# Kernel tuning notes

Hardware: AMD Instinct MI355X
Metric: run time of the kernel (lower is better)

Reference implementation:

```python
import jax, jax.numpy as jnp
import numpy as np

N_NODES = 50000
N_EDGES = 1600000
IN_DIM = 128
HID = 64
H1 = 2          # heads layer 0
H2 = 1          # heads layer 1
N_CLS = 16
NEG_SLOPE = 0.2


def setup_inputs() -> dict:
    key = jax.random.key(0)
    ks = jax.random.split(key, 10)
    h = jax.random.normal(ks[0], (N_NODES, IN_DIM), dtype=jnp.float32)
    src = jax.random.randint(ks[1], (N_EDGES,), 0, N_NODES, dtype=jnp.int64)
    dst = jax.random.randint(ks[2], (N_EDGES,), 0, N_NODES, dtype=jnp.int64)
    s = 0.05
    W1_src = jax.random.normal(ks[3], (IN_DIM, H1 * HID), dtype=jnp.float32) * s
    W1_dst = jax.random.normal(ks[4], (IN_DIM, H1 * HID), dtype=jnp.float32) * s
    a1 = jax.random.normal(ks[5], (H1, HID), dtype=jnp.float32) * s
    W2_src = jax.random.normal(ks[6], (H1 * HID, H2 * N_CLS), dtype=jnp.float32) * s
    W2_dst = jax.random.normal(ks[7], (H1 * HID, H2 * N_CLS), dtype=jnp.float32) * s
    a2 = jax.random.normal(ks[8], (H2, N_CLS), dtype=jnp.float32) * s
    W_res = jax.random.normal(ks[9], (H1 * HID, H2 * N_CLS), dtype=jnp.float32) * s
    return {"h": h, "src": src, "dst": dst, "W1_src": W1_src, "W1_dst": W1_dst,
            "a1": a1, "W2_src": W2_src, "W2_dst": W2_dst, "a2": a2, "W_res": W_res}


def _gatv2_conv(h, src, dst, W_src, W_dst, attn, n_nodes):
    # GATv2: e_ij = a . LeakyReLU(W_src h_j + W_dst h_i), softmax over in-edges of i
    heads, out_dim = attn.shape
    fs = (h @ W_src).reshape(-1, heads, out_dim)  # [N,H,D]
    fd = (h @ W_dst).reshape(-1, heads, out_dim)
    e = jax.nn.leaky_relu(fs[src] + fd[dst], negative_slope=NEG_SLOPE)  # [E,H,D]
    score = jnp.einsum('ehd,hd->eh', e, attn)                           # [E,H]
    m = jax.ops.segment_max(score, dst, num_segments=n_nodes)           # [N,H]
    ex = jnp.exp(score - m[dst])
    denom = jax.ops.segment_sum(ex, dst, num_segments=n_nodes)          # [N,H]
    alpha = ex / denom[dst]                                             # [E,H]
    msg = alpha[:, :, None] * fs[src]                                   # [E,H,D]
    return jax.ops.segment_sum(msg, dst, num_segments=n_nodes)          # [N,H,D]


def reference(h, src, dst, W1_src, W1_dst, a1, W2_src, W2_dst, a2, W_res):
    n = h.shape[0]
    # layer 0: GATv2Conv -> elu activation -> flatten heads
    h1 = _gatv2_conv(h, src, dst, W1_src, W1_dst, a1, n)   # [N,H1,HID]
    h1 = jax.nn.elu(h1).reshape(n, -1)                      # [N,H1*HID]
    # layer 1: GATv2Conv with residual, no activation, mean over heads
    h2 = _gatv2_conv(h1, src, dst, W2_src, W2_dst, a2, n)   # [N,H2,N_CLS]
    res = (h1 @ W_res).reshape(n, H2, N_CLS)
    logits = (h2 + res).mean(axis=1)                        # [N,N_CLS]
    return logits
```

## Files before the change

### kernel.cpp

```cpp
#include <hip/hip_runtime.h>
#include <hip/hip_bf16.h>

#define NEG 0.2f
#define FNEG_MAX -3.402823466e38f

__device__ __forceinline__ unsigned short f2bf(float f){
  unsigned u = __float_as_uint(f);
  return (unsigned short)((u + 0x7fffu + ((u >> 16) & 1u)) >> 16);
}
__device__ __forceinline__ unsigned pk2bf(float a, float b){
  return (unsigned)f2bf(a) | ((unsigned)f2bf(b) << 16);
}
__device__ __forceinline__ float bflo(unsigned u){ return __uint_as_float(u << 16); }
__device__ __forceinline__ float bfhi(unsigned u){ return __uint_as_float(u & 0xffff0000u); }

__global__ __launch_bounds__(256)
void k_count(const int* __restrict__ dst, int* __restrict__ deg, int ne){
  int e = blockIdx.x*256 + threadIdx.x;
  if (e < ne) atomicAdd(&deg[dst[e]], 1);
}

#define SCB 512
__global__ __launch_bounds__(SCB)
void k_scan1(const int* __restrict__ deg, int* __restrict__ off,
             int* __restrict__ bsum, int n){
  __shared__ int lds[SCB];
  int t = threadIdx.x, i = blockIdx.x*SCB + t;
  int x = (i < n) ? deg[i] : 0;
  lds[t] = x; __syncthreads();
  for (int s = 1; s < SCB; s <<= 1){
    int v = (t >= s) ? lds[t-s] : 0;
    __syncthreads();
    lds[t] += v;
    __syncthreads();
  }
  if (i < n) off[i] = lds[t] - x;
  if (t == SCB-1) bsum[blockIdx.x] = lds[t];
}

__global__ void k_scan2(int* __restrict__ bsum, int nblk){
  if (threadIdx.x == 0 && blockIdx.x == 0){
    int acc = 0;
    for (int b = 0; b < nblk; ++b){ int v = bsum[b]; bsum[b] = acc; acc += v; }
  }
}

__global__ __launch_bounds__(SCB)
void k_scan3(int* __restrict__ off, const int* __restrict__ bsum, int n, int ne){
  int i = blockIdx.x*SCB + threadIdx.x;
  if (i < n) off[i] += bsum[blockIdx.x];
  if (i == 0) off[n] = ne;
}

__global__ __launch_bounds__(256)
void k_scatter(const int* __restrict__ src, const int* __restrict__ dst,
               const int* __restrict__ off, int* __restrict__ cur,
               int* __restrict__ csr_src, int ne){
  int e = blockIdx.x*256 + threadIdx.x;
  if (e >= ne) return;
  int d = dst[e];
  int pos = off[d] + atomicAdd(&cur[d], 1);
  csr_src[pos] = src[e];
}

#define GM1 32
__global__ __launch_bounds__(256)
void k_gemm1(const float* __restrict__ h, const float* __restrict__ Ws,
             const float* __restrict__ Wd, unsigned* __restrict__ fs,
             float* __restrict__ fd, int n){
  __shared__ float ht[128][36];
  int tid = threadIdx.x;
  int node0 = blockIdx.x * GM1;
  for (int i = tid; i < GM1*128; i += 256){
    int r = i >> 7, c = i & 127;
    int nd = node0 + r;
    ht[c][r] = (nd < n) ? h[(size_t)nd*128 + c] : 0.f;
  }
  __syncthreads();
  int cg  = tid & 31;
  int mat = (tid >> 5) & 1;
  int q   = tid >> 6;
  const float4* W4 = (const float4*)(mat ? Wd : Ws);
  float acc[8][4];
  #pragma unroll
  for (int j = 0; j < 8; ++j){ acc[j][0]=0.f; acc[j][1]=0.f; acc[j][2]=0.f; acc[j][3]=0.f; }
  for (int k = 0; k < 128; ++k){
    float4 w = W4[k*32 + cg];
    const float4* hp4 = (const float4*)&ht[k][q*8];
    float4 ha = hp4[0], hb = hp4[1];
    float hv[8] = {ha.x, ha.y, ha.z, ha.w, hb.x, hb.y, hb.z, hb.w};
    #pragma unroll
    for (int j = 0; j < 8; ++j){
      acc[j][0] = fmaf(hv[j], w.x, acc[j][0]);
      acc[j][1] = fmaf(hv[j], w.y, acc[j][1]);
      acc[j][2] = fmaf(hv[j], w.z, acc[j][2]);
      acc[j][3] = fmaf(hv[j], w.w, acc[j][3]);
    }
  }
  #pragma unroll
  for (int j = 0; j < 8; ++j){
    int nd = node0 + q*8 + j;
    if (nd < n){
      if (mat == 0){
        uint2 o; o.x = pk2bf(acc[j][0], acc[j][1]); o.y = pk2bf(acc[j][2], acc[j][3]);
        ((uint2*)fs)[(size_t)nd*32 + cg] = o;
      } else {
        float4 o; o.x=acc[j][0]; o.y=acc[j][1]; o.z=acc[j][2]; o.w=acc[j][3];
        ((float4*)fd)[(size_t)nd*32 + cg] = o;
      }
    }
  }
}

#define THR1 10.f
__global__ __launch_bounds__(256)
void k_l1_node(const unsigned* __restrict__ fs, const float* fdv_,
               const int* __restrict__ off, const int* __restrict__ csr,
               const float* __restrict__ a1, float* out, int n){
  int wid  = (int)((blockIdx.x*256u + threadIdx.x) >> 6);
  int lane = threadIdx.x & 63;
  if (wid >= n) return;
  int d  = wid;
  int hh = lane >> 5;
  int lp = lane & 31;
  int e0 = off[d], e1 = off[d+1];
  int deg = e1 - e0;
  const uint2* fs2v = (const uint2*)fs;
  float4 fdv = ((const float4*)fdv_)[(size_t)d*32 + lp];
  float4 aw  = ((const float4*)a1)[lp];
  float m = FNEG_MAX, den = 0.f;
  float4 acc = make_float4(0.f, 0.f, 0.f, 0.f);

  int nt = (deg + 3) & ~3;
  for (int k = 0; k < nt; k += 4){
    int eiA = e0 + k + hh;
    int eiB = eiA + 2;
    bool vA = eiA < e1, vB = eiB < e1;
    int sA = csr[vA ? eiA : e0];
    int sB = csr[vB ? eiB : e0];
    uint2 uA = fs2v[(size_t)sA*32 + lp];
    uint2 uB = fs2v[(size_t)sB*32 + lp];
    float xA0 = bflo(uA.x), xA1 = bfhi(uA.x), xA2 = bflo(uA.y), xA3 = bfhi(uA.y);
    float xB0 = bflo(uB.x), xB1 = bfhi(uB.x), xB2 = bflo(uB.y), xB3 = bfhi(uB.y);
    float pA, pB;
    {
      float t0 = xA0 + fdv.x, t1 = xA1 + fdv.y;
      float t2 = xA2 + fdv.z, t3 = xA3 + fdv.w;
      t0 = fmaxf(t0, NEG*t0); t1 = fmaxf(t1, NEG*t1);
      t2 = fmaxf(t2, NEG*t2); t3 = fmaxf(t3, NEG*t3);
      pA = fmaf(t0, aw.x, fmaf(t1, aw.y, fmaf(t2, aw.z, t3*aw.w)));
    }
    {
      float t0 = xB0 + fdv.x, t1 = xB1 + fdv.y;
      float t2 = xB2 + fdv.z, t3 = xB3 + fdv.w;
      t0 = fmaxf(t0, NEG*t0); t1 = fmaxf(t1, NEG*t1);
      t2 = fmaxf(t2, NEG*t2); t3 = fmaxf(t3, NEG*t3);
      pB = fmaf(t0, aw.x, fmaf(t1, aw.y, fmaf(t2, aw.z, t3*aw.w)));
    }
    #pragma unroll
    for (int o = 8; o >= 1; o >>= 1){
      pA += __shfl_xor(pA, o, 64);
      pB += __shfl_xor(pB, o, 64);
    }
    pA = vA ? pA : FNEG_MAX;
    pB = vB ? pB : FNEG_MAX;
    float pmax = fmaxf(pA, pB);
    if (__any(pmax > m + THR1)){
      float nm = fmaxf(m, pmax);
      float sc = __expf(m - nm);
      den *= sc;
      acc.x *= sc; acc.y *= sc; acc.z *= sc; acc.w *= sc;
      m = nm;
    }
    float wA = vA ? __expf(pA - m) : 0.f;
    float wB = vB ? __expf(pB - m) : 0.f;
    den += wA + wB;
    acc.x = fmaf(wA, xA0, fmaf(wB, xB0, acc.x));
    acc.y = fmaf(wA, xA1, fmaf(wB, xB1, acc.y));
    acc.z = fmaf(wA, xA2, fmaf(wB, xB2, acc.z));
    acc.w = fmaf(wA, xA3, fmaf(wB, xB3, acc.w));
  }

  float om   = __shfl_xor(m,   32, 64);
  float oden = __shfl_xor(den, 32, 64);
  float4 oacc;
  oacc.x = __shfl_xor(acc.x, 32, 64);
  oacc.y = __shfl_xor(acc.y, 32, 64);
  oacc.z = __shfl_xor(acc.z, 32, 64);
  oacc.w = __shfl_xor(acc.w, 32, 64);
  float nm = fmaxf(m, om);
  float s1 = __expf(m - nm), s2 = __expf(om - nm);
  den = den*s1 + oden*s2;
  float4 r;
  r.x = acc.x*s1 + oacc.x*s2;
  r.y = acc.y*s1 + oacc.y*s2;
  r.z = acc.z*s1 + oacc.z*s2;
  r.w = acc.w*s1 + oacc.w*s2;
  float inv = (den > 0.f) ? 1.f/den : 0.f;
  r.x *= inv; r.y *= inv; r.z *= inv; r.w *= inv;
  r.x = r.x > 0.f ? r.x : __expf(r.x) - 1.f;
  r.y = r.y > 0.f ? r.y : __expf(r.y) - 1.f;
  r.z = r.z > 0.f ? r.z : __expf(r.z) - 1.f;
  r.w = r.w > 0.f ? r.w : __expf(r.w) - 1.f;
  if (hh == 0) ((float4*)out)[(size_t)d*32 + lp] = r;
}

__global__ __launch_bounds__(256)
void k_gemm2(const float* __restrict__ h1, const float* __restrict__ Ws,
             const float* __restrict__ Wd, const float* __restrict__ Wr,
             unsigned short* __restrict__ fs2, float* __restrict__ fd2,
             float* __restrict__ res, int n){
  __shared__ float hs[16][129];
  __shared__ float w[3][128][16];
  int tid = threadIdx.x;
  for (int i = tid; i < 2048; i += 256){
    int k = i >> 4, j = i & 15;
    w[0][k][j] = Ws[i]; w[1][k][j] = Wd[i]; w[2][k][j] = Wr[i];
  }
  int node0 = blockIdx.x * 16;
  for (int i = tid; i < 2048; i += 256){
    int r = i >> 7, c = i & 127;
    int nd = node0 + r;
    hs[r][c] = (nd < n) ? h1[(size_t)nd*128 + c] : 0.f;
  }
  __syncthreads();
  int j = tid & 15, ni = tid >> 4;
  float as = 0.f, ad = 0.f, ar = 0.f;
  for (int k = 0; k < 128; ++k){
    float hv = hs[ni][k];
    as = fmaf(hv, w[0][k][j], as);
    ad = fmaf(hv, w[1][k][j], ad);
    ar = fmaf(hv, w[2][k][j], ar);
  }
  int nd = node0 + ni;
  if (nd < n){
    fs2[(size_t)nd*16 + j] = f2bf(as);
    fd2[(size_t)nd*16 + j] = ad;
    res[(size_t)nd*16 + j] = ar;
  }
}

#define THR2 10.f
__global__ __launch_bounds__(256)
void k_l2_node(const unsigned short* __restrict__ fs2, const float* __restrict__ fd2,
               const float* __restrict__ resd, const int* __restrict__ off,
               const int* __restrict__ csr, const float* __restrict__ a2,
               float* __restrict__ outp, int n){
  int wid  = (int)((blockIdx.x*256u + threadIdx.x) >> 6);
  int lane = threadIdx.x & 63;
  if (wid >= n) return;
  int d = wid;
  int g = lane >> 4, j = lane & 15;
  int e0 = off[d], e1 = off[d+1];
  int deg = e1 - e0;
  float fdv = fd2[(size_t)d*16 + j];
  float aw  = a2[j];
  float m = FNEG_MAX, den = 0.f, acc = 0.f;
  int jmax = (deg + 7) >> 3;
  for (int it = 0; it < jmax; ++it){
    int iA = e0 + it*8 + g;
    int iB = iA + 4;
    bool vA = iA < e1, vB = iB < e1;
    int sA = csr[vA ? iA : e0];
    int sB = csr[vB ? iB : e0];
    float xA = __uint_as_float((unsigned)fs2[(size_t)sA*16 + j] << 16);
    float xB = __uint_as_float((unsigned)fs2[(size_t)sB*16 + j] << 16);
    float tA = xA + fdv; tA = fmaxf(tA, NEG*tA);
    float tB = xB + fdv; tB = fmaxf(tB, NEG*tB);
    float pA = tA * aw, pB = tB * aw;
    #pragma unroll
    for (int o = 8; o >= 1; o >>= 1){
      pA += __shfl_xor(pA, o, 64);
      pB += __shfl_xor(pB, o, 64);
    }
    pA = vA ? pA : FNEG_MAX;
    pB = vB ? pB : FNEG_MAX;
    float pmax = fmaxf(pA, pB);
    if (__any(pmax > m + THR2)){
      float nm = fmaxf(m, pmax);
      float sc = __expf(m - nm);
      den *= sc; acc *= sc;
      m = nm;
    }
    float wA = vA ? __expf(pA - m) : 0.f;
    float wB = vB ? __expf(pB - m) : 0.f;
    den += wA + wB;
    acc = fmaf(wA, xA, fmaf(wB, xB, acc));
  }
  #pragma unroll
  for (int o = 16; o <= 32; o <<= 1){
    float om   = __shfl_xor(m,   o, 64);
    float oden = __shfl_xor(den, o, 64);
    float oacc = __shfl_xor(acc, o, 64);
    float nm = fmaxf(m, om);
    float s1 = __expf(m - nm);
    float s2 = __expf(om - nm);
    den = den*s1 + oden*s2;
    acc = acc*s1 + oacc*s2;
    m = nm;
  }
  if (g == 0){
    float inv = (den > 0.f) ? 1.f/den : 0.f;
    outp[(size_t)d*16 + j] = acc*inv + resd[(size_t)d*16 + j];
  }
}

extern "C" void kernel_launch(void* const* d_in, const int* in_sizes, int n_in,
                              void* d_out, int out_size, void* d_ws, size_t ws_size,
                              hipStream_t stream) {
  const float* h    = (const float*)d_in[0];
  const int*   src  = (const int*)  d_in[1];
  const int*   dst  = (const int*)  d_in[2];
  const float* W1s  = (const float*)d_in[3];
  const float* W1d  = (const float*)d_in[4];
  const float* a1   = (const float*)d_in[5];
  const float* W2s  = (const float*)d_in[6];
  const float* W2d  = (const float*)d_in[7];
  const float* a2   = (const float*)d_in[8];
  const float* Wres = (const float*)d_in[9];
  float* out = (float*)d_out;

  const int n  = in_sizes[0] / 128;
  const int ne = in_sizes[1];

  float* ws  = (float*)d_ws;
  float* fs1 = ws;
  float* fd1 = fs1 + (size_t)n*128;
  float* fs2 = fd1 + (size_t)n*128;
  float* fd2 = fs2 + (size_t)n*16;
  float* res = fd2 + (size_t)n*16;
  int* deg     = (int*)(res + (size_t)n*16);
  int* off     = deg + n;
  int* cur     = off + (n+1);
  int* bsum    = cur + n;
  int* csr_src = bsum + 128;

  const int nblk = (n + SCB - 1) / SCB;

  hipMemsetAsync(deg, 0, (size_t)n*4, stream);
  hipMemsetAsync(cur, 0, (size_t)n*4, stream);
  k_count  <<<(ne + 255)/256, 256, 0, stream>>>(dst, deg, ne);
  k_scan1  <<<nblk, SCB, 0, stream>>>(deg, off, bsum, n);
  k_scan2  <<<1, 64, 0, stream>>>(bsum, nblk);
  k_scan3  <<<nblk, SCB, 0, stream>>>(off, bsum, n, ne);
  k_scatter<<<(ne + 255)/256, 256, 0, stream>>>(src, dst, off, cur, csr_src, ne);

  k_gemm1  <<<(n + GM1 - 1)/GM1, 256, 0, stream>>>(h, W1s, W1d, (unsigned*)fs1, fd1, n);
  k_l1_node<<<(n + 3)/4, 256, 0, stream>>>((const unsigned*)fs1, fd1, off, csr_src, a1, fd1, n);

  k_gemm2  <<<(n + 15)/16, 256, 0, stream>>>(fd1, W2s, W2d, Wres, (unsigned short*)fs2, fd2, res, n);
  k_l2_node<<<(n + 3)/4, 256, 0, stream>>>((const unsigned short*)fs2, fd2, res, off, csr_src, a2, out, n);
}
```

Baseline: 374.6 us.

## Merge CSR scan into single-block kernel and fuse scatter with first GEMM

The three-kernel prefix scan becomes one 1024-thread single-block scan that also zeroes the cursor array, which removes a memset and two launches. The edge scatter into CSR is folded into the first projection GEMM launch as extra blocks, so the latency-bound scatter and the compute-bound GEMM can run concurrently. The cost is a serial per-thread chunk scan (about 49 elements per thread) running on one CU, and GEMM blocks now share the machine with the atomic scatter blocks.

```diff
diff --git a/kernel.cpp b/kernel.cpp
--- a/kernel.cpp
+++ b/kernel.cpp
@@ -20,56 +20,52 @@
   if (e < ne) atomicAdd(&deg[dst[e]], 1);
 }
 
-#define SCB 512
-__global__ __launch_bounds__(SCB)
-void k_scan1(const int* __restrict__ deg, int* __restrict__ off,
-             int* __restrict__ bsum, int n){
-  __shared__ int lds[SCB];
-  int t = threadIdx.x, i = blockIdx.x*SCB + t;
-  int x = (i < n) ? deg[i] : 0;
-  lds[t] = x; __syncthreads();
-  for (int s = 1; s < SCB; s <<= 1){
-    int v = (t >= s) ? lds[t-s] : 0;
+__global__ __launch_bounds__(1024)
+void k_scan(const int* __restrict__ deg, int* __restrict__ off,
+            int* __restrict__ cur, int n, int ne){
+  __shared__ int lds[1024];
+  int t = threadIdx.x;
+  int per = (n + 1023) >> 10;
+  int base = t * per;
+  int end = base + per; if (end > n) end = n;
+  int s = 0;
+  for (int i = base; i < end; ++i) s += deg[i];
+  lds[t] = s;
+  __syncthreads();
+  for (int o = 1; o < 1024; o <<= 1){
+    int v = (t >= o) ? lds[t - o] : 0;
     __syncthreads();
     lds[t] += v;
     __syncthreads();
   }
-  if (i < n) off[i] = lds[t] - x;
-  if (t == SCB-1) bsum[blockIdx.x] = lds[t];
-}
-
-__global__ void k_scan2(int* __restrict__ bsum, int nblk){
-  if (threadIdx.x == 0 && blockIdx.x == 0){
-    int acc = 0;
-    for (int b = 0; b < nblk; ++b){ int v = bsum[b]; bsum[b] = acc; acc += v; }
-  }
-}
-
-__global__ __launch_bounds__(SCB)
-void k_scan3(int* __restrict__ off, const int* __restrict__ bsum, int n, int ne){
-  int i = blockIdx.x*SCB + threadIdx.x;
-  if (i < n) off[i] += bsum[blockIdx.x];
-  if (i == 0) off[n] = ne;
-}
-
-__global__ __launch_bounds__(256)
-void k_scatter(const int* __restrict__ src, const int* __restrict__ dst,
-               const int* __restrict__ off, int* __restrict__ cur,
-               int* __restrict__ csr_src, int ne){
-  int e = blockIdx.x*256 + threadIdx.x;
-  if (e >= ne) return;
-  int d = dst[e];
-  int pos = off[d] + atomicAdd(&cur[d], 1);
-  csr_src[pos] = src[e];
+  int run = lds[t] - s;
+  for (int i = base; i < end; ++i){
+    off[i] = run;
+    run += deg[i];
+    cur[i] = 0;
+  }
+  if (t == 0) off[n] = ne;
 }
 
 #define GM1 32
 __global__ __launch_bounds__(256)
-void k_gemm1(const float* __restrict__ h, const float* __restrict__ Ws,
-             const float* __restrict__ Wd, unsigned* __restrict__ fs,
-             float* __restrict__ fd, int n){
+void k_gemm1_scatter(const float* __restrict__ h, const float* __restrict__ Ws,
+                     const float* __restrict__ Wd, unsigned* __restrict__ fs,
+                     float* __restrict__ fd,
+                     const int* __restrict__ src, const int* __restrict__ dst,
+                     const int* __restrict__ off, int* __restrict__ cur,
+                     int* __restrict__ csr_src, int n, int ne, int nbg){
   __shared__ float ht[128][36];
   int tid = threadIdx.x;
+  if ((int)blockIdx.x >= nbg){
+    int e = ((int)blockIdx.x - nbg)*256 + tid;
+    if (e < ne){
+      int d = dst[e];
+      int pos = off[d] + atomicAdd(&cur[d], 1);
+      csr_src[pos] = src[e];
+    }
+    return;
+  }
   int node0 = blockIdx.x * GM1;
   for (int i = tid; i < GM1*128; i += 256){
     int r = i >> 7, c = i & 127;
@@ -335,17 +331,16 @@
   int* bsum    = cur + n;
   int* csr_src = bsum + 128;
 
-  const int nblk = (n + SCB - 1) / SCB;
+  const int nbg = (n + GM1 - 1) / GM1;
+  const int nbs = (ne + 255) / 256;
 
   hipMemsetAsync(deg, 0, (size_t)n*4, stream);
-  hipMemsetAsync(cur, 0, (size_t)n*4, stream);
-  k_count  <<<(ne + 255)/256, 256, 0, stream>>>(dst, deg, ne);
-  k_scan1  <<<nblk, SCB, 0, stream>>>(deg, off, bsum, n);
-  k_scan2  <<<1, 64, 0, stream>>>(bsum, nblk);
-  k_scan3  <<<nblk, SCB, 0, stream>>>(off, bsum, n, ne);
-  k_scatter<<<(ne + 255)/256, 256, 0, stream>>>(src, dst, off, cur, csr_src, ne);
-
-  k_gemm1  <<<(n + GM1 - 1)/GM1, 256, 0, stream>>>(h, W1s, W1d, (unsigned*)fs1, fd1, n);
+  k_count<<<(ne + 255)/256, 256, 0, stream>>>(dst, deg, ne);
+  k_scan <<<1, 1024, 0, stream>>>(deg, off, cur, n, ne);
+
+  k_gemm1_scatter<<<nbg + nbs, 256, 0, stream>>>(
+      h, W1s, W1d, (unsigned*)fs1, fd1, src, dst, off, cur,
+      csr_src, n, ne, nbg);
   k_l1_node<<<(n + 3)/4, 256, 0, stream>>>((const unsigned*)fs1, fd1, off, csr_src, a1, fd1, n);
 
   k_gemm2  <<<(n + 15)/16, 256, 0, stream>>>(fd1, W2s, W2d, Wres, (unsigned short*)fs2, fd2, res, n);
```

Result: slower. 413.5 us (+10.4%).
